# Performance work log

Measured on AMD Instinct MI355X. Metric: run time of the kernel, lower is better.

## Reference

```python
import jax, jax.numpy as jnp
import numpy as np

B, C, H, W = 4, 512, 64, 64
CQ = C // 8


def setup_inputs() -> dict:
    key = jax.random.key(0)
    k1, k2, k3, k4, k5 = jax.random.split(key, 5)
    return {
        "x": jax.random.normal(k1, (B, C, H, W), dtype=jnp.float32),
        "Wq": jax.random.normal(k2, (CQ, C), dtype=jnp.float32) * (2.0 / C) ** 0.5,
        "Wk": jax.random.normal(k3, (CQ, C), dtype=jnp.float32) * (2.0 / C) ** 0.5,
        "Wv": jax.random.normal(k4, (C, C), dtype=jnp.float32) * (2.0 / C) ** 0.5,
        "gamma": jax.random.normal(k5, (1,), dtype=jnp.float32),
    }


def reference(x, Wq, Wk, Wv, gamma):
    b, c, h, w = x.shape
    n = h * w
    xf = x.reshape(b, c, n)                       # (B, C, N)
    # 1x1 convs (bias=False, norm=identity) == channel matmuls
    q = jnp.einsum('qc,bcn->bnq', Wq, xf)         # (B, N, Cq) -- proj_query permuted
    k = jnp.einsum('qc,bcm->bqm', Wk, xf)         # (B, Cq, N) -- proj_key
    energy = jnp.einsum('bnq,bqm->bnm', q, k)     # (B, N, N)
    attn = jax.nn.softmax(energy, axis=-1)        # softmax over keys (last dim)
    v = jnp.einsum('dc,bcm->bdm', Wv, xf)         # (B, C, N) -- proj_value
    # out = bmm(V, attn^T): out[b,d,n] = sum_m V[b,d,m] * attn[b,n,m]
    out = jnp.einsum('bdm,bnm->bdn', v, attn).reshape(b, c, h, w)
    return gamma * out + x
```

## Files before the change

### kernel.cpp

```cpp
#include <hip/hip_runtime.h>

#define B_  4
#define C_  512
#define CQ_ 64
#define N_  4096
#define LOG2E 1.44269504088896f

typedef _Float16 half8 __attribute__((ext_vector_type(8)));
typedef _Float16 half4 __attribute__((ext_vector_type(4)));
typedef float    f32x4 __attribute__((ext_vector_type(4)));

__device__ __forceinline__ void g2l16(const void* g, void* l) {
  __builtin_amdgcn_global_load_lds(
      (const __attribute__((address_space(1))) void*)g,
      (__attribute__((address_space(3))) void*)l, 16, 0, 0);
}

__global__ __launch_bounds__(256) void wcvt_kernel(
    const float* __restrict__ Wq, const float* __restrict__ Wk,
    const float* __restrict__ Wv, _Float16* __restrict__ Wh)
{
  const int row = blockIdx.x;
  const float* src;
  float s = 1.0f;
  if (row < 64)       { src = Wq + (size_t)row * C_; s = LOG2E; }
  else if (row < 128) { src = Wk + (size_t)(row - 64) * C_; }
  else                { src = Wv + (size_t)(row - 128) * C_; }
  for (int c = threadIdx.x; c < C_; c += 256)
    Wh[(size_t)row * C_ + c] = (_Float16)(src[c] * s);
}

__global__ __launch_bounds__(256) void proj_kernel(
    const float* __restrict__ x, const _Float16* __restrict__ Wh,
    _Float16* __restrict__ Qh, _Float16* __restrict__ Kh, _Float16* __restrict__ Vh)
{
  __shared__ _Float16 xs[32][520];
  __shared__ _Float16 vs[64][40];

  const int tid = threadIdx.x;
  const int wid = tid >> 6, lane = tid & 63, ln = lane & 15, lh = lane >> 4;

  const int wg = (blockIdx.x & 7) * 64 + (blockIdx.x >> 3);
  const int b  = wg >> 7;
  const int n0 = (wg & 127) * 32;

  {
    const int nn = (tid & 7) * 4;
    const int c0 = tid >> 3;
    #pragma unroll 4
    for (int cc = 0; cc < 16; ++cc) {
      const int c = cc * 32 + c0;
      f32x4 v = *(const f32x4*)&x[((size_t)b * C_ + c) * N_ + n0 + nn];
      #pragma unroll
      for (int u = 0; u < 4; ++u) xs[nn + u][c] = (_Float16)v[u];
    }
  }
  __syncthreads();

  for (int chT = 0; chT < 10; ++chT) {
    f32x4 acc[2] = {};
    const _Float16* wrow = Wh + (size_t)(chT * 64 + wid * 16 + ln) * C_;

    #pragma unroll 4
    for (int kt = 0; kt < C_; kt += 32) {
      half8 a = *(const half8*)&wrow[kt + lh * 8];
      #pragma unroll
      for (int ct = 0; ct < 2; ++ct) {
        half8 bf = *(const half8*)&xs[ct * 16 + ln][kt + lh * 8];
        acc[ct] = __builtin_amdgcn_mfma_f32_16x16x32_f16(a, bf, acc[ct], 0, 0, 0);
      }
    }

    if (chT < 2) {
      #pragma unroll
      for (int ct = 0; ct < 2; ++ct) {
        const int n = n0 + ct * 16 + ln;
        #pragma unroll
        for (int j = 0; j < 4; ++j) {
          const int chL = wid * 16 + lh * 4 + j;
          const _Float16 v = (_Float16)acc[ct][j];
          if (chT == 0) Qh[((size_t)b * N_ + n) * CQ_ + chL] = v;
          else          Kh[((size_t)b * N_ + n) * CQ_ + chL] = v;
        }
      }
    } else {
      __syncthreads();
      #pragma unroll
      for (int ct = 0; ct < 2; ++ct)
        #pragma unroll
        for (int j = 0; j < 4; ++j)
          vs[wid * 16 + lh * 4 + j][ct * 16 + ln] = (_Float16)acc[ct][j];
      __syncthreads();
      const int row = tid >> 2, cb = (tid & 3) * 8;
      *(half8*)&Vh[((size_t)b * C_ + (chT - 2) * 64 + row) * N_ + n0 + cb] =
          *(const half8*)&vs[row][cb];
    }
  }
}

__global__ __launch_bounds__(512, 2) void stats_kernel(
    const _Float16* __restrict__ Qh, const _Float16* __restrict__ Kh,
    float* __restrict__ m_g, float* __restrict__ il_g)
{
  __shared__ float Ms[8][64];
  __shared__ float Ss[8][64];

  const int tid = threadIdx.x;
  const int wid = tid >> 6, lane = tid & 63, ln = lane & 15, lh = lane >> 4;
  const int b  = blockIdx.x >> 6;
  const int qb = (blockIdx.x & 63) * 64;

  half8 qf[4][2];
  #pragma unroll
  for (int rt = 0; rt < 4; ++rt)
    #pragma unroll
    for (int h = 0; h < 2; ++h)
      qf[rt][h] = *(const half8*)&Qh[((size_t)b * N_ + qb + rt * 16 + ln) * CQ_ + h * 32 + lh * 8];

  float mx[4] = {-3.0e38f, -3.0e38f, -3.0e38f, -3.0e38f};
  float sm[4] = {0.f, 0.f, 0.f, 0.f};

  const _Float16* kp = Kh + ((size_t)b * N_ + wid * 16 + ln) * CQ_ + lh * 8;

  half8 k0 = *(const half8*)kp;
  half8 k1 = *(const half8*)(kp + 32);

  for (int it = 0; it < 32; ++it) {
    half8 kn0, kn1;
    if (it < 31) {
      const _Float16* kq = kp + (size_t)((it + 1) * 128) * CQ_;
      kn0 = *(const half8*)kq;
      kn1 = *(const half8*)(kq + 32);
    }
    #pragma unroll
    for (int rt = 0; rt < 4; ++rt) {
      f32x4 e = {};
      e = __builtin_amdgcn_mfma_f32_16x16x32_f16(k0, qf[rt][0], e, 0, 0, 0);
      e = __builtin_amdgcn_mfma_f32_16x16x32_f16(k1, qf[rt][1], e, 0, 0, 0);
      const float m1 = fmaxf(fmaxf(e[0], e[1]), fmaxf(e[2], e[3]));
      const float mn = fmaxf(mx[rt], m1);
      sm[rt] = sm[rt] * exp2f(mx[rt] - mn)
             + exp2f(e[0] - mn) + exp2f(e[1] - mn)
             + exp2f(e[2] - mn) + exp2f(e[3] - mn);
      mx[rt] = mn;
    }
    k0 = kn0; k1 = kn1;
  }

  #pragma unroll
  for (int rt = 0; rt < 4; ++rt) {
    float m = mx[rt], s = sm[rt];
    #pragma unroll
    for (int mask = 16; mask <= 32; mask <<= 1) {
      const float om = __shfl_xor(m, mask);
      const float os = __shfl_xor(s, mask);
      const float mn = fmaxf(m, om);
      s = s * exp2f(m - mn) + os * exp2f(om - mn);
      m = mn;
    }
    if (lane < 16) { Ms[wid][rt * 16 + lane] = m; Ss[wid][rt * 16 + lane] = s; }
  }
  __syncthreads();
  if (tid < 64) {
    float m = Ms[0][tid], s = Ss[0][tid];
    #pragma unroll
    for (int w = 1; w < 8; ++w) {
      const float om = Ms[w][tid], os = Ss[w][tid];
      const float mn = fmaxf(m, om);
      s = s * exp2f(m - mn) + os * exp2f(om - mn);
      m = mn;
    }
    m_g[(size_t)b * N_ + qb + tid]  = m;
    il_g[(size_t)b * N_ + qb + tid] = 1.0f / s;
  }
}

__global__ __launch_bounds__(512) void fpv_kernel(
    const float* __restrict__ x, const _Float16* __restrict__ Qh,
    const _Float16* __restrict__ Kh, const _Float16* __restrict__ Vh,
    const float* __restrict__ m_g, const float* __restrict__ il_g,
    const float* __restrict__ gamma, float* __restrict__ out)
{
  __shared__ _Float16 As[3][256 * 64];
  __shared__ _Float16 Ks[3][64 * 64];
  __shared__ _Float16 Ps[128 * 64];

  const int tid = threadIdx.x;
  const int wid = tid >> 6, lane = tid & 63, ln = lane & 15, lh = lane >> 4;

  const int wg = (blockIdx.x & 7) * 32 + (blockIdx.x >> 3);
  const int dt = wg & 1;
  const int nt = (wg >> 1) & 31;
  const int b  = wg >> 6;
  const int d0 = dt * 256, n0 = nt * 128;

  const float m2  = m_g [(size_t)b * N_ + n0 + wid * 16 + ln];
  const float il2 = il_g[(size_t)b * N_ + n0 + wid * 16 + ln];

  half8 qf[2];
  #pragma unroll
  for (int h = 0; h < 2; ++h)
    qf[h] = *(const half8*)&Qh[((size_t)b * N_ + n0 + wid * 16 + ln) * CQ_ + h * 32 + lh * 8];

  const int srow   = lane >> 3;
  const int schunk = lane & 7;
  const _Float16* aSrc[4];
  #pragma unroll
  for (int r = 0; r < 4; ++r) {
    const int row = r * 64 + wid * 8 + srow;
    aSrc[r] = Vh + ((size_t)b * C_ + d0 + row) * N_ + ((schunk ^ (row & 7)) << 3);
  }
  const _Float16* kSrc;
  {
    const int row = wid * 8 + srow;
    kSrc = Kh + ((size_t)b * N_ + row) * CQ_ + ((schunk ^ (row & 7)) << 3);
  }

  auto stage = [&](int buf, int t) {
    const int mA = t << 6;
    #pragma unroll
    for (int r = 0; r < 4; ++r)
      g2l16(aSrc[r] + mA, (char*)&As[buf][0] + r * 8192 + wid * 1024);
    g2l16(kSrc + (size_t)(t << 6) * CQ_, (char*)&Ks[buf][0] + wid * 1024);
  };

  const int dr = wid >> 1, nc = wid & 1;
  const int swl = ln & 7;
  f32x4 acc[4][4] = {};

  stage(0, 0);
  stage(1, 1);

  for (int t = 0; t < 64; ++t) {
    if (t < 63) { asm volatile("s_waitcnt vmcnt(5)" ::: "memory"); }
    else        { asm volatile("s_waitcnt vmcnt(0)" ::: "memory"); }
    __builtin_amdgcn_s_barrier();
    __builtin_amdgcn_sched_barrier(0);

    const int buf = t % 3;

    {
      const _Float16* Kr = &Ks[buf][0];
      half8 kf[4][2];
      #pragma unroll
      for (int kt = 0; kt < 4; ++kt) {
        const int key = kt * 16 + ln;
        #pragma unroll
        for (int c = 0; c < 2; ++c)
          kf[kt][c] = *(const half8*)&Kr[key * 64 + ((((c << 2) | lh) ^ swl) << 3)];
      }

      if (t < 62) stage((t + 2) % 3, t + 2);

      #pragma unroll
      for (int kt = 0; kt < 4; ++kt) {
        f32x4 e = {};
        e = __builtin_amdgcn_mfma_f32_16x16x32_f16(kf[kt][0], qf[0], e, 0, 0, 0);
        e = __builtin_amdgcn_mfma_f32_16x16x32_f16(kf[kt][1], qf[1], e, 0, 0, 0);
        half4 pv;
        #pragma unroll
        for (int j = 0; j < 4; ++j)
          pv[j] = (_Float16)(exp2f(e[j] - m2) * il2);
        *(half4*)((char*)&Ps[(wid * 16 + ln) * 64]
                  + ((((kt << 1) | (lh >> 1)) ^ swl) << 4) + ((lh & 1) << 3)) = pv;
      }
    }

    asm volatile("s_waitcnt lgkmcnt(0)" ::: "memory");
    __builtin_amdgcn_sched_barrier(0);
    __builtin_amdgcn_s_barrier();
    __builtin_amdgcn_sched_barrier(0);

    {
      const _Float16* Ar = &As[buf][0];
      half8 a[4][2], bq[4][2];
      #pragma unroll
      for (int ft = 0; ft < 4; ++ft) {
        const int row = dr * 64 + ft * 16 + ln;
        #pragma unroll
        for (int c = 0; c < 2; ++c)
          a[ft][c] = *(const half8*)&Ar[row * 64 + ((((c << 2) | lh) ^ swl) << 3)];
      }
      #pragma unroll
      for (int gt = 0; gt < 4; ++gt) {
        const int q = nc * 64 + gt * 16 + ln;
        #pragma unroll
        for (int c = 0; c < 2; ++c)
          bq[gt][c] = *(const half8*)&Ps[q * 64 + ((((c << 2) | lh) ^ swl) << 3)];
      }
      #pragma unroll
      for (int c = 0; c < 2; ++c)
        #pragma unroll
        for (int ft = 0; ft < 4; ++ft)
          #pragma unroll
          for (int gt = 0; gt < 4; ++gt)
            acc[ft][gt] = __builtin_amdgcn_mfma_f32_16x16x32_f16(a[ft][c], bq[gt][c], acc[ft][gt], 0, 0, 0);
    }
  }

  const float g = gamma[0];
  #pragma unroll
  for (int ft = 0; ft < 4; ++ft) {
    #pragma unroll
    for (int gt = 0; gt < 4; ++gt) {
      #pragma unroll
      for (int j = 0; j < 4; ++j) {
        const int d = d0 + dr * 64 + ft * 16 + lh * 4 + j;
        const int n = n0 + nc * 64 + gt * 16 + ln;
        const size_t idx = ((size_t)b * C_ + d) * N_ + n;
        out[idx] = g * acc[ft][gt][j] + x[idx];
      }
    }
  }
}

extern "C" void kernel_launch(void* const* d_in, const int* in_sizes, int n_in,
                              void* d_out, int out_size, void* d_ws, size_t ws_size,
                              hipStream_t stream) {
  const float* x     = (const float*)d_in[0];
  const float* Wq    = (const float*)d_in[1];
  const float* Wk    = (const float*)d_in[2];
  const float* Wv    = (const float*)d_in[3];
  const float* gamma = (const float*)d_in[4];
  float* out = (float*)d_out;

  _Float16* Qh = (_Float16*)d_ws;
  _Float16* Kh = Qh + (size_t)B_ * N_ * CQ_;
  _Float16* Vh = Kh + (size_t)B_ * N_ * CQ_;
  float* m_g   = (float*)(Vh + (size_t)B_ * C_ * N_);
  float* il_g  = m_g + (size_t)B_ * N_;
  _Float16* Wh = (_Float16*)(il_g + (size_t)B_ * N_);

  wcvt_kernel<<<dim3(640), 256, 0, stream>>>(Wq, Wk, Wv, Wh);
  proj_kernel<<<dim3(512), 256, 0, stream>>>(x, Wh, Qh, Kh, Vh);
  stats_kernel<<<dim3(256), 512, 0, stream>>>(Qh, Kh, m_g, il_g);
  fpv_kernel<<<dim3(256), 512, 0, stream>>>(x, Qh, Kh, Vh, m_g, il_g, gamma, out);
}
```

Baseline: 195.2 us.

## Warp-specialize attention kernel into P producers and PV consumers with register-staged V

```diff
diff --git a/kernel.cpp b/kernel.cpp
--- a/kernel.cpp
+++ b/kernel.cpp
@@ -175,18 +175,18 @@
   }
 }
 
-__global__ __launch_bounds__(512) void fpv_kernel(
+__global__ __launch_bounds__(512) void fpv2_kernel(
     const float* __restrict__ x, const _Float16* __restrict__ Qh,
     const _Float16* __restrict__ Kh, const _Float16* __restrict__ Vh,
     const float* __restrict__ m_g, const float* __restrict__ il_g,
     const float* __restrict__ gamma, float* __restrict__ out)
 {
-  __shared__ _Float16 As[3][256 * 64];
   __shared__ _Float16 Ks[3][64 * 64];
-  __shared__ _Float16 Ps[128 * 64];
+  __shared__ _Float16 Ps[2][128 * 64];
 
   const int tid = threadIdx.x;
   const int wid = tid >> 6, lane = tid & 63, ln = lane & 15, lh = lane >> 4;
+  const bool prod = (wid < 4);
 
   const int wg = (blockIdx.x & 7) * 32 + (blockIdx.x >> 3);
   const int dt = wg & 1;
@@ -194,121 +194,127 @@
   const int b  = wg >> 6;
   const int d0 = dt * 256, n0 = nt * 128;
 
-  const float m2  = m_g [(size_t)b * N_ + n0 + wid * 16 + ln];
-  const float il2 = il_g[(size_t)b * N_ + n0 + wid * 16 + ln];
-
-  half8 qf[2];
+  const int swl = ln & 7;
+
+  const int krow = tid >> 3;
+  const int kch  = (tid & 7) ^ (krow & 7);
+  const _Float16* kSrc = Kh + ((size_t)b * N_ + krow) * CQ_ + (kch << 3);
+
+  const int pq = prod ? wid * 32 : 0;
+  float m2[2], il2[2];
+  half8 qf[2][2];
   #pragma unroll
-  for (int h = 0; h < 2; ++h)
-    qf[h] = *(const half8*)&Qh[((size_t)b * N_ + n0 + wid * 16 + ln) * CQ_ + h * 32 + lh * 8];
-
-  const int srow   = lane >> 3;
-  const int schunk = lane & 7;
-  const _Float16* aSrc[4];
-  #pragma unroll
-  for (int r = 0; r < 4; ++r) {
-    const int row = r * 64 + wid * 8 + srow;
-    aSrc[r] = Vh + ((size_t)b * C_ + d0 + row) * N_ + ((schunk ^ (row & 7)) << 3);
-  }
-  const _Float16* kSrc;
-  {
-    const int row = wid * 8 + srow;
-    kSrc = Kh + ((size_t)b * N_ + row) * CQ_ + ((schunk ^ (row & 7)) << 3);
-  }
-
-  auto stage = [&](int buf, int t) {
-    const int mA = t << 6;
-    #pragma unroll
-    for (int r = 0; r < 4; ++r)
-      g2l16(aSrc[r] + mA, (char*)&As[buf][0] + r * 8192 + wid * 1024);
-    g2l16(kSrc + (size_t)(t << 6) * CQ_, (char*)&Ks[buf][0] + wid * 1024);
-  };
-
-  const int dr = wid >> 1, nc = wid & 1;
-  const int swl = ln & 7;
-  f32x4 acc[4][4] = {};
-
-  stage(0, 0);
-  stage(1, 1);
-
-  for (int t = 0; t < 64; ++t) {
-    if (t < 63) { asm volatile("s_waitcnt vmcnt(5)" ::: "memory"); }
-    else        { asm volatile("s_waitcnt vmcnt(0)" ::: "memory"); }
+  for (int rt = 0; rt < 2; ++rt) {
+    const size_t qidx = (size_t)b * N_ + n0 + pq + rt * 16 + ln;
+    m2[rt]  = m_g [qidx];
+    il2[rt] = il_g[qidx];
+    #pragma unroll
+    for (int h = 0; h < 2; ++h)
+      qf[rt][h] = *(const half8*)&Qh[qidx * CQ_ + h * 32 + lh * 8];
+  }
+
+  const int v64 = prod ? 0 : (wid - 4) * 64;
+  const _Float16* vBase = Vh + ((size_t)b * C_ + d0 + v64 + ln) * (size_t)N_ + (lh << 3);
+  half8 vc[4][2];
+  f32x4 acc[4][8] = {};
+
+  g2l16(kSrc,                        (char*)&Ks[0][0] + wid * 1024);
+  g2l16(kSrc + (size_t)64 * CQ_,     (char*)&Ks[1][0] + wid * 1024);
+  if (!prod) {
+    #pragma unroll
+    for (int ft = 0; ft < 4; ++ft)
+      #pragma unroll
+      for (int c = 0; c < 2; ++c)
+        vc[ft][c] = *(const half8*)(vBase + (size_t)ft * 16 * N_ + c * 32);
+  }
+
+  for (int t = 0; t <= 64; ++t) {
+    if (prod) { asm volatile("s_waitcnt vmcnt(1)" ::: "memory"); }
+    else      { asm volatile("s_waitcnt vmcnt(9)" ::: "memory"); }
     __builtin_amdgcn_s_barrier();
     __builtin_amdgcn_sched_barrier(0);
 
-    const int buf = t % 3;
-
-    {
-      const _Float16* Kr = &Ks[buf][0];
-      half8 kf[4][2];
-      #pragma unroll
-      for (int kt = 0; kt < 4; ++kt) {
-        const int key = kt * 16 + ln;
-        #pragma unroll
-        for (int c = 0; c < 2; ++c)
-          kf[kt][c] = *(const half8*)&Kr[key * 64 + ((((c << 2) | lh) ^ swl) << 3)];
-      }
-
-      if (t < 62) stage((t + 2) % 3, t + 2);
-
-      #pragma unroll
-      for (int kt = 0; kt < 4; ++kt) {
-        f32x4 e = {};
-        e = __builtin_amdgcn_mfma_f32_16x16x32_f16(kf[kt][0], qf[0], e, 0, 0, 0);
-        e = __builtin_amdgcn_mfma_f32_16x16x32_f16(kf[kt][1], qf[1], e, 0, 0, 0);
-        half4 pv;
-        #pragma unroll
-        for (int j = 0; j < 4; ++j)
-          pv[j] = (_Float16)(exp2f(e[j] - m2) * il2);
-        *(half4*)((char*)&Ps[(wid * 16 + ln) * 64]
-                  + ((((kt << 1) | (lh >> 1)) ^ swl) << 4) + ((lh & 1) << 3)) = pv;
-      }
-    }
-
-    asm volatile("s_waitcnt lgkmcnt(0)" ::: "memory");
-    __builtin_amdgcn_sched_barrier(0);
-    __builtin_amdgcn_s_barrier();
-    __builtin_amdgcn_sched_barrier(0);
-
-    {
-      const _Float16* Ar = &As[buf][0];
-      half8 a[4][2], bq[4][2];
-      #pragma unroll
-      for (int ft = 0; ft < 4; ++ft) {
-        const int row = dr * 64 + ft * 16 + ln;
-        #pragma unroll
-        for (int c = 0; c < 2; ++c)
-          a[ft][c] = *(const half8*)&Ar[row * 64 + ((((c << 2) | lh) ^ swl) << 3)];
-      }
-      #pragma unroll
-      for (int gt = 0; gt < 4; ++gt) {
-        const int q = nc * 64 + gt * 16 + ln;
-        #pragma unroll
-        for (int c = 0; c < 2; ++c)
-          bq[gt][c] = *(const half8*)&Ps[q * 64 + ((((c << 2) | lh) ^ swl) << 3)];
-      }
-      #pragma unroll
-      for (int c = 0; c < 2; ++c)
-        #pragma unroll
-        for (int ft = 0; ft < 4; ++ft)
-          #pragma unroll
-          for (int gt = 0; gt < 4; ++gt)
-            acc[ft][gt] = __builtin_amdgcn_mfma_f32_16x16x32_f16(a[ft][c], bq[gt][c], acc[ft][gt], 0, 0, 0);
-    }
-  }
-
-  const float g = gamma[0];
-  #pragma unroll
-  for (int ft = 0; ft < 4; ++ft) {
-    #pragma unroll
-    for (int gt = 0; gt < 4; ++gt) {
-      #pragma unroll
-      for (int j = 0; j < 4; ++j) {
-        const int d = d0 + dr * 64 + ft * 16 + lh * 4 + j;
-        const int n = n0 + nc * 64 + gt * 16 + ln;
-        const size_t idx = ((size_t)b * C_ + d) * N_ + n;
-        out[idx] = g * acc[ft][gt][j] + x[idx];
+    if (t < 62)
+      g2l16(kSrc + (size_t)(t + 2) * 64 * CQ_, (char*)&Ks[(t + 2) % 3][0] + wid * 1024);
+
+    if (prod) {
+      if (t < 64) {
+        const _Float16* Kr = &Ks[t % 3][0];
+        half8 kf[4][2];
+        #pragma unroll
+        for (int kt = 0; kt < 4; ++kt) {
+          const int key = kt * 16 + ln;
+          #pragma unroll
+          for (int c = 0; c < 2; ++c)
+            kf[kt][c] = *(const half8*)&Kr[key * 64 + ((((c << 2) | lh) ^ swl) << 3)];
+        }
+        _Float16* Pw = &Ps[t & 1][0];
+        #pragma unroll
+        for (int rt = 0; rt < 2; ++rt) {
+          #pragma unroll
+          for (int kt = 0; kt < 4; ++kt) {
+            f32x4 e = {};
+            e = __builtin_amdgcn_mfma_f32_16x16x32_f16(kf[kt][0], qf[rt][0], e, 0, 0, 0);
+            e = __builtin_amdgcn_mfma_f32_16x16x32_f16(kf[kt][1], qf[rt][1], e, 0, 0, 0);
+            half4 pv;
+            #pragma unroll
+            for (int j = 0; j < 4; ++j)
+              pv[j] = (_Float16)(exp2f(e[j] - m2[rt]) * il2[rt]);
+            *(half4*)((char*)&Pw[(pq + rt * 16 + ln) * 64]
+                      + ((((kt << 1) | (lh >> 1)) ^ swl) << 4) + ((lh & 1) << 3)) = pv;
+          }
+        }
+        asm volatile("s_waitcnt lgkmcnt(0)" ::: "memory");
+        __builtin_amdgcn_sched_barrier(0);
+      }
+    } else {
+      if (t >= 1) {
+        half8 vn[4][2];
+        if (t < 64) {
+          const _Float16* vp = vBase + (size_t)t * 64;
+          #pragma unroll
+          for (int ft = 0; ft < 4; ++ft)
+            #pragma unroll
+            for (int c = 0; c < 2; ++c)
+              vn[ft][c] = *(const half8*)(vp + (size_t)ft * 16 * N_ + c * 32);
+        }
+
+        const _Float16* Pr = &Ps[(t - 1) & 1][0];
+        #pragma unroll
+        for (int c = 0; c < 2; ++c) {
+          #pragma unroll
+          for (int gt = 0; gt < 8; ++gt) {
+            half8 bq = *(const half8*)&Pr[(gt * 16 + ln) * 64 + ((((c << 2) | lh) ^ swl) << 3)];
+            #pragma unroll
+            for (int ft = 0; ft < 4; ++ft)
+              acc[ft][gt] = __builtin_amdgcn_mfma_f32_16x16x32_f16(vc[ft][c], bq, acc[ft][gt], 0, 0, 0);
+          }
+        }
+
+        if (t < 64) {
+          #pragma unroll
+          for (int ft = 0; ft < 4; ++ft)
+            #pragma unroll
+            for (int c = 0; c < 2; ++c)
+              vc[ft][c] = vn[ft][c];
+        }
+      }
+    }
+  }
+
+  if (!prod) {
+    const float g = gamma[0];
+    #pragma unroll
+    for (int ft = 0; ft < 4; ++ft) {
+      #pragma unroll
+      for (int gt = 0; gt < 8; ++gt) {
+        #pragma unroll
+        for (int j = 0; j < 4; ++j) {
+          const int d = d0 + v64 + ft * 16 + lh * 4 + j;
+          const int n = n0 + gt * 16 + ln;
+          const size_t idx = ((size_t)b * C_ + d) * N_ + n;
+          out[idx] = g * acc[ft][gt][j] + x[idx];
+        }
       }
     }
   }
@@ -334,5 +340,5 @@
   wcvt_kernel<<<dim3(640), 256, 0, stream>>>(Wq, Wk, Wv, Wh);
   proj_kernel<<<dim3(512), 256, 0, stream>>>(x, Wh, Qh, Kh, Vh);
   stats_kernel<<<dim3(256), 512, 0, stream>>>(Qh, Kh, m_g, il_g);
-  fpv_kernel<<<dim3(256), 512, 0, stream>>>(x, Qh, Kh, Vh, m_g, il_g, gamma, out);
-}
+  fpv2_kernel<<<dim3(256), 512, 0, stream>>>(x, Qh, Kh, Vh, m_g, il_g, gamma, out);
+}
```

Result: slower. 214.4 us (+9.8%).
